# Performance work log

Hardware: AMD Instinct MI355X
Metric: run time of the kernel (lower is better)

## Reference

```python
import jax, jax.numpy as jnp
import numpy as np

# Dimensions (babyGPT-50m: GPT-2-small-ish)
B, T, V, C, H, L = 2, 1024, 50257, 768, 12, 6
D = C // H
STD = 0.02
EPS = 1e-5


def _normal(k, shape):
    return (jax.random.normal(k, shape, dtype=jnp.float32) * STD)


def setup_inputs() -> dict:
    key = jax.random.key(0)
    ks = jax.random.split(key, 12)
    inp = {
        "idx": jax.random.randint(ks[0], (B, T), 0, V, dtype=jnp.int64 if jax.config.jax_enable_x64 else jnp.int32),
        "tok_emb": _normal(ks[1], (V, C)),
        "pos_emb": _normal(ks[2], (1, T, C)),
        # per-layer params stacked along leading L axis
        "ln1_g": jnp.ones((L, C), jnp.float32),
        "ln1_b": jnp.zeros((L, C), jnp.float32),
        "Wq": _normal(ks[3], (L, C, C)), "bq": jnp.zeros((L, C), jnp.float32),
        "Wk": _normal(ks[4], (L, C, C)), "bk": jnp.zeros((L, C), jnp.float32),
        "Wv": _normal(ks[5], (L, C, C)), "bv": jnp.zeros((L, C), jnp.float32),
        "Wp": _normal(ks[6], (L, C, C)), "bp": jnp.zeros((L, C), jnp.float32),
        "ln2_g": jnp.ones((L, C), jnp.float32),
        "ln2_b": jnp.zeros((L, C), jnp.float32),
        "Wf1": _normal(ks[7], (L, C, 4 * C)), "bf1": jnp.zeros((L, 4 * C), jnp.float32),
        "Wf2": _normal(ks[8], (L, 4 * C, C)), "bf2": jnp.zeros((L, C), jnp.float32),
        "lnf_g": jnp.ones((C,), jnp.float32),
        "lnf_b": jnp.zeros((C,), jnp.float32),
        "head_W": _normal(ks[9], (C, V)),  # head has bias=False
    }
    return inp


def _ln(x, g, b):
    m = jnp.mean(x, axis=-1, keepdims=True)
    v = jnp.var(x, axis=-1, keepdims=True)
    return (x - m) * jax.lax.rsqrt(v + EPS) * g + b


def _gpt_forward(idx, tok_emb, pos_emb, ln1_g, ln1_b, Wq, bq, Wk, bk, Wv, bv,
                 Wp, bp, ln2_g, ln2_b, Wf1, bf1, Wf2, bf2, lnf_g, lnf_b, head_W):
    x = tok_emb[idx] + pos_emb[:, :T]          # [B,T,C]; dropout is identity (eval)
    causal = jnp.tril(jnp.ones((T, T), bool))  # same tril mask as the buffer
    scale = 1.0 / np.sqrt(D).astype(np.float32)

    def block(x, p):
        g1, b1, wq, bq_, wk, bk_, wv, bv_, wp, bp_, g2, b2, w1, b1f, w2, b2f = p
        h = _ln(x, g1, b1)
        q = (h @ wq + bq_).reshape(B, T, H, D)
        k = (h @ wk + bk_).reshape(B, T, H, D)
        v = (h @ wv + bv_).reshape(B, T, H, D)
        att = jnp.einsum('bthd,bshd->bhts', q, k) * scale   # [B,H,T,T]
        att = jnp.where(causal, att, jnp.float32(-10000.0))  # masked_fill value
        att = jax.nn.softmax(att, axis=-1)
        y = jnp.einsum('bhts,bshd->bthd', att, v).reshape(B, T, C)
        x = x + y @ wp + bp_
        h2 = _ln(x, g2, b2)
        ff = jax.nn.gelu(h2 @ w1 + b1f, approximate=False) @ w2 + b2f  # exact GELU, dropout=eval
        return x + ff, None

    layer_params = (ln1_g, ln1_b, Wq, bq, Wk, bk, Wv, bv, Wp, bp,
                    ln2_g, ln2_b, Wf1, bf1, Wf2, bf2)
    x, _ = jax.lax.scan(block, x, layer_params)
    x = _ln(x, lnf_g, lnf_b)
    return x @ head_W  # logits [B,T,V]


def reference(idx, tok_emb, pos_emb, ln1_g, ln1_b, Wq, bq, Wk, bk, Wv, bv,
              Wp, bp, ln2_g, ln2_b, Wf1, bf1, Wf2, bf2, lnf_g, lnf_b, head_W):
    return _gpt_forward(idx, tok_emb, pos_emb, ln1_g, ln1_b, Wq, bq, Wk, bk, Wv, bv,
                        Wp, bp, ln2_g, ln2_b, Wf1, bf1, Wf2, bf2, lnf_g, lnf_b, head_W)
```

## Files before the change

kernel.cpp:

```cpp
#include <hip/hip_runtime.h>
#include <hip/hip_bf16.h>
#include <math.h>

#define Bsz 2
#define Tt 1024
#define Vv 50257
#define Cc 768
#define Hh 12
#define Ll 6
#define NTOK (Bsz*Tt)
#define VPAD 50304

typedef __attribute__((ext_vector_type(8))) short bf16x8;
typedef __attribute__((ext_vector_type(8))) unsigned short u16x8;
typedef __attribute__((ext_vector_type(4))) unsigned short u16x4;
typedef __attribute__((ext_vector_type(4))) float f32x4;
typedef unsigned short u16;

static __device__ __forceinline__ u16 f2bf(float f){
  unsigned u = __float_as_uint(f);
  u += 0x7FFF + ((u >> 16) & 1);
  return (u16)(u >> 16);
}
static __device__ __forceinline__ float bf2f(u16 h){
  return __uint_as_float(((unsigned)h) << 16);
}

#define GL16(g,l) __builtin_amdgcn_global_load_lds( \
    (const __attribute__((address_space(1))) void*)(g), \
    (__attribute__((address_space(3))) void*)(l), 16, 0, 0)
#define WAITVM(n) asm volatile("s_waitcnt vmcnt(%0)" :: "n"(n) : "memory")

__global__ void embed_kernel(const int* __restrict__ idx, const float* __restrict__ tok,
                             const float* __restrict__ pos, float* __restrict__ x){
  const int C4 = Cc/4;
  int i = blockIdx.x * 256 + threadIdx.x;
  if (i >= NTOK*C4) return;
  int tk = i / C4, c4 = i % C4;
  int row = idx[tk];
  int t = tk % Tt;
  float4 a = ((const float4*)tok)[(size_t)row*C4 + c4];
  float4 p = ((const float4*)pos)[(size_t)t*C4 + c4];
  float4 r; r.x=a.x+p.x; r.y=a.y+p.y; r.z=a.z+p.z; r.w=a.w+p.w;
  ((float4*)x)[i] = r;
}

__global__ void ln_kernel(const float* __restrict__ in, const float* __restrict__ g,
                          const float* __restrict__ bt, u16* __restrict__ out){
  int row = blockIdx.x, tid = threadIdx.x;
  const float* r = in + (size_t)row*Cc;
  float v0=r[tid], v1=r[tid+256], v2=r[tid+512];
  float s  = v0+v1+v2;
  float s2 = v0*v0+v1*v1+v2*v2;
  #pragma unroll
  for (int off=32; off; off>>=1){ s += __shfl_xor(s,off); s2 += __shfl_xor(s2,off); }
  __shared__ float red[8];
  int wid = tid >> 6;
  if ((tid & 63) == 0){ red[wid]=s; red[4+wid]=s2; }
  __syncthreads();
  float S  = red[0]+red[1]+red[2]+red[3];
  float S2 = red[4]+red[5]+red[6]+red[7];
  float mean = S * (1.0f/Cc);
  float var  = S2 * (1.0f/Cc) - mean*mean;
  float rstd = rsqrtf(var + 1e-5f);
  u16* o = out + (size_t)row*Cc;
  o[tid]     = f2bf((v0-mean)*rstd*g[tid]     + bt[tid]);
  o[tid+256] = f2bf((v1-mean)*rstd*g[tid+256] + bt[tid+256]);
  o[tid+512] = f2bf((v2-mean)*rstd*g[tid+512] + bt[tid+512]);
}

__global__ void wtrans_kernel(const float* __restrict__ in, u16* __restrict__ out,
                              int K, int N, int Npad, size_t lsi, size_t lso){
  __shared__ u16 t[64][68];
  const float* inp = in + (size_t)blockIdx.z*lsi;
  u16* op = out + (size_t)blockIdx.z*lso;
  int n0 = blockIdx.x*64, k0 = blockIdx.y*64;
  int tid = threadIdx.x;
  #pragma unroll
  for (int i=0;i<4;i++){
    int e = tid + 256*i;
    int k = e >> 4, n4 = (e & 15) * 4;
    int n = n0 + n4;
    const float* rowp = inp + (size_t)(k0+k)*N;
    float4 v;
    if (n + 3 < N) v = *(const float4*)&rowp[n];
    else {
      v.x = (n   < N) ? rowp[n  ] : 0.f;
      v.y = (n+1 < N) ? rowp[n+1] : 0.f;
      v.z = (n+2 < N) ? rowp[n+2] : 0.f;
      v.w = (n+3 < N) ? rowp[n+3] : 0.f;
    }
    u16x4 pk; pk[0]=f2bf(v.x); pk[1]=f2bf(v.y); pk[2]=f2bf(v.z); pk[3]=f2bf(v.w);
    *(u16x4*)&t[k][n4] = pk;
  }
  __syncthreads();
  #pragma unroll
  for (int i=0;i<2;i++){
    int e = tid + 256*i;
    int n = e >> 3, k8 = (e & 7) * 8;
    u16x8 pk;
    #pragma unroll
    for (int q=0;q<8;q++) pk[q] = t[k8+q][n];
    if (n0 + n < Npad)
      *(u16x8*)&op[(size_t)(n0+n)*K + k0 + k8] = pk;
  }
}

__global__ void vtrans_kernel(const u16* __restrict__ qkv, u16* __restrict__ vT){
  __shared__ u16 s[32][33];
  int bh = blockIdx.z; int b = bh/Hh, h = bh - b*Hh;
  int t0 = blockIdx.x*32, d0 = blockIdx.y*32;
  int tx=threadIdx.x, ty=threadIdx.y;
  #pragma unroll
  for (int i=0;i<4;i++)
    s[ty+i*8][tx] = qkv[(size_t)(b*Tt + t0+ty+i*8)*2304 + 1536 + h*64 + d0 + tx];
  __syncthreads();
  #pragma unroll
  for (int i=0;i<4;i++)
    vT[((size_t)bh*64 + d0+ty+i*8)*Tt + t0 + tx] = s[tx][ty+i*8];
}

__global__ void bconcat_kernel(const float* __restrict__ bq, const float* __restrict__ bk,
                               const float* __restrict__ bv, float* __restrict__ o){
  int i = blockIdx.x*256 + threadIdx.x;
  if (i >= Ll*2304) return;
  int l = i/2304, j = i - l*2304;
  o[i] = (j < 768) ? bq[l*768+j] : (j < 1536) ? bk[l*768+j-768] : bv[l*768+j-1536];
}

__global__ __launch_bounds__(256) void flash_kernel(
    const u16* __restrict__ qkv, const u16* __restrict__ vT, u16* __restrict__ y){
  __shared__ u16 Ks[2][64*64];
  __shared__ u16 Vs[2][64*64];
  __shared__ u16 Ps[4][16*64];
  int bx = blockIdx.x;
  int bh = blockIdx.y; int b = bh/Hh, h = bh - b*Hh;
  int q0 = bx*64;
  int tid = threadIdx.x, lane = tid&63, wid = tid>>6;
  const size_t tokbase = (size_t)b*Tt;
  int arow = lane&15, akof = (lane>>4)*8;
  bf16x8 qa[2];
  #pragma unroll
  for (int ks=0;ks<2;ks++)
    qa[ks] = *(const bf16x8*)&qkv[(tokbase + q0 + wid*16 + arow)*2304
                                  + h*64 + ks*32 + akof];
  int srow = lane>>3;
  int sbyte = ((lane&7)*16) ^ (srow<<4);
  const u16* kbase = qkv + tokbase*2304 + 768 + h*64;
  const u16* vbase = vT + (size_t)bh*64*Tt;
  auto STAGEKV = [&](int t, int bb){
    int j0 = t*64;
    #pragma unroll
    for (int c=0;c<2;c++){
      int r = wid*16 + c*8 + srow;
      GL16(kbase + (size_t)(j0 + r)*2304 + (sbyte>>1), &Ks[bb][(wid*16 + c*8)*64]);
      GL16(vbase + (size_t)r*Tt + j0 + (sbyte>>1),     &Vs[bb][(wid*16 + c*8)*64]);
    }
  };
  float m_r[4], l_r[4];
  f32x4 o_acc[4] = {};
  #pragma unroll
  for (int jj=0;jj<4;jj++){ m_r[jj] = -1e30f; l_r[jj] = 0.f; }

  int njt = bx + 1;
  STAGEKV(0, 0);
  asm volatile("s_waitcnt vmcnt(0)" ::: "memory");
  __builtin_amdgcn_s_barrier();
  for (int t=0; t<njt; t++){
    int cur = t&1;
    if (t+1 < njt) STAGEKV(t+1, cur^1);
    int j0 = t*64;
    f32x4 sacc[4] = {};
    #pragma unroll
    for (int ks=0;ks<2;ks++){
      bf16x8 kf[4];
      #pragma unroll
      for (int ni=0;ni<4;ni++){
        int s16 = ni*16 + (lane&15);
        int kb = (ks*64 + (lane>>4)*16) ^ ((s16&7)<<4);
        kf[ni] = *(const bf16x8*)((const char*)&Ks[cur][0] + s16*128 + kb);
      }
      #pragma unroll
      for (int ni=0;ni<4;ni++)
        sacc[ni] = __builtin_amdgcn_mfma_f32_16x16x32_bf16(qa[ks], kf[ni], sacc[ni], 0,0,0);
    }
    float tmax[4];
    #pragma unroll
    for (int jj=0;jj<4;jj++) tmax[jj] = -1e30f;
    #pragma unroll
    for (int ni=0;ni<4;ni++)
      #pragma unroll
      for (int jj=0;jj<4;jj++){
        float v = sacc[ni][jj]*0.125f;
        int sg = j0 + ni*16 + (lane&15);
        int tg = q0 + wid*16 + (lane>>4)*4 + jj;
        v = (sg <= tg) ? v : -1e30f;
        sacc[ni][jj] = v;
        tmax[jj] = fmaxf(tmax[jj], v);
      }
    #pragma unroll
    for (int jj=0;jj<4;jj++){
      float tm = tmax[jj];
      tm = fmaxf(tm, __shfl_xor(tm,1)); tm = fmaxf(tm, __shfl_xor(tm,2));
      tm = fmaxf(tm, __shfl_xor(tm,4)); tm = fmaxf(tm, __shfl_xor(tm,8));
      float mn = fmaxf(m_r[jj], tm);
      float al = __expf(m_r[jj] - mn);
      m_r[jj] = mn;
      l_r[jj] *= al;
      tmax[jj] = al;
    }
    float tsum[4] = {};
    #pragma unroll
    for (int ni=0;ni<4;ni++)
      #pragma unroll
      for (int jj=0;jj<4;jj++){
        float p = __expf(sacc[ni][jj] - m_r[jj]);
        tsum[jj] += p;
        int pr = (lane>>4)*4 + jj;
        int pcb = (2*(ni*16 + (lane&15))) ^ ((pr&7)<<4);
        *(u16*)((char*)&Ps[wid][0] + pr*128 + pcb) = f2bf(p);
      }
    #pragma unroll
    for (int jj=0;jj<4;jj++){
      float ts = tsum[jj];
      ts += __shfl_xor(ts,1); ts += __shfl_xor(ts,2);
      ts += __shfl_xor(ts,4); ts += __shfl_xor(ts,8);
      l_r[jj] += ts;
      float al = tmax[jj];
      #pragma unroll
      for (int ni2=0;ni2<4;ni2++) o_acc[ni2][jj] *= al;
    }
    #pragma unroll
    for (int ks2=0;ks2<2;ks2++){
      bf16x8 pa, vf[4];
      int prr = lane&15;
      int pb = (ks2*64 + (lane>>4)*16) ^ ((prr&7)<<4);
      pa = *(const bf16x8*)((const char*)&Ps[wid][0] + prr*128 + pb);
      #pragma unroll
      for (int ni2=0;ni2<4;ni2++){
        int d16 = ni2*16 + (lane&15);
        int sb = (ks2*64 + (lane>>4)*16) ^ ((d16&7)<<4);
        vf[ni2] = *(const bf16x8*)((const char*)&Vs[cur][0] + d16*128 + sb);
      }
      #pragma unroll
      for (int ni2=0;ni2<4;ni2++)
        o_acc[ni2] = __builtin_amdgcn_mfma_f32_16x16x32_bf16(pa, vf[ni2], o_acc[ni2], 0,0,0);
    }
    asm volatile("s_waitcnt vmcnt(0) lgkmcnt(0)" ::: "memory");
    __builtin_amdgcn_s_barrier();
  }
  #pragma unroll
  for (int jj=0;jj<4;jj++){
    float inv = 1.0f / l_r[jj];
    int tok2 = q0 + wid*16 + (lane>>4)*4 + jj;
    size_t rb = (tokbase + tok2)*Cc + h*64;
    #pragma unroll
    for (int ni2=0;ni2<4;ni2++)
      y[rb + ni2*16 + (lane&15)] = f2bf(o_acc[ni2][jj] * inv);
  }
}

template<int NBUF, int NTHR, int WN, int BM, int BN, int BK,
         bool BIAS, bool RESID, bool GELU, bool OUTBF, bool ROWSCAN>
__global__ __launch_bounds__(NTHR) void mm_kernel(
    const u16* __restrict__ A, const u16* __restrict__ Bm,
    const float* __restrict__ bias, const float* __restrict__ resid,
    void* __restrict__ out, int N, int K, int lda, int ldb, int ldc)
{
  constexpr int WAVES = NTHR/64;
  constexpr int WM    = WAVES/WN;
  constexpr int FM    = BM/(WM*16);
  constexpr int FN    = BN/(WN*16);
  constexpr int KSTEPS = BK/32;
  constexpr int CPW   = FN*16;
  constexpr int ESTR  = CPW + 4;
  constexpr int ABUF  = BM*BK;
  constexpr int BBUF  = BN*BK;
  constexpr int ARPW  = BM/WAVES;
  constexpr int BRPW  = BN/WAVES;
  constexpr int RPC   = (BK==64) ? 8 : 16;
  constexpr int ACALLS = ARPW/RPC;
  constexpr int BCALLS = BRPW/RPC;
  constexpr int LOADS = ACALLS + BCALLS;
  constexpr int SMEM_STAGE = NBUF*(ABUF+BBUF)*2;
  constexpr int SMEM_EPI   = WAVES*16*ESTR*4;
  constexpr int SMEMB = SMEM_STAGE > SMEM_EPI ? SMEM_STAGE : SMEM_EPI;
  __shared__ __align__(16) char smem[SMEMB];
  u16* As = (u16*)smem;
  u16* Bs = As + NBUF*ABUF;

  int bx = blockIdx.x, by = blockIdx.y;
  {
    int gx = gridDim.x;
    int nwg = gx * gridDim.y;
    int flat = by*gx + bx;
    int qq = nwg >> 3, rr = nwg & 7;
    int xcd = flat & 7, lid = flat >> 3;
    int swz = (xcd < rr) ? xcd*(qq+1) + lid : rr*(qq+1) + (xcd-rr)*qq + lid;
    bx = swz % gx; by = swz / gx;
  }
  int m0 = bx*BM, n0 = by*BN;
  int tid = threadIdx.x, lane = tid & 63, wid = tid >> 6;
  int r0 = (wid/WN)*(BM/WM), c0 = (wid%WN)*(BN/WN);
  int lrow = lane & 15;
  int rl, sswz;
  if constexpr (BK==64){ rl = lane>>3; sswz = ((lane&7) ^ (lane>>3)) * 8; }
  else                 { rl = lane>>2; sswz = ((lane&3) ^ ((lane>>3)&3)) * 8; }
  const u16* Ap = A + (size_t)(m0 + wid*ARPW + rl)*lda + sswz;
  const u16* Bp = Bm + (size_t)(n0 + wid*BRPW + rl)*ldb + sswz;
  int nt = K/BK;
  auto STAGE = [&](int t, int bb){
    int kk = t*BK;
    u16* Al = As + bb*ABUF + (wid*ARPW)*BK;
    #pragma unroll
    for (int c=0;c<ACALLS;c++)
      GL16(Ap + kk + (size_t)(c*RPC)*lda, Al + c*512);
    u16* Bl = Bs + bb*BBUF + (wid*BRPW)*BK;
    #pragma unroll
    for (int c=0;c<BCALLS;c++)
      GL16(Bp + kk + (size_t)(c*RPC)*ldb, Bl + c*512);
  };
  f32x4 acc[FM][FN] = {};
  if constexpr (NBUF==2){
    STAGE(0, 0);
    WAITVM(0);
    __builtin_amdgcn_s_barrier();
  } else {
    STAGE(0, 0);
    if (nt > 1) STAGE(1, 1);
    WAITVM(LOADS);
    __builtin_amdgcn_s_barrier();
  }
  for (int t = 0; t < nt; t++){
    int bb = (NBUF==2) ? (t & 1) : (t % 3);
    if constexpr (NBUF==2){
      if (t+1 < nt) STAGE(t+1, (t+1)&1);
    } else {
      if (t+2 < nt) STAGE(t+2, (t+2)%3);
    }
    const char* Ab2 = (const char*)(As + bb*ABUF);
    const char* Bb2 = (const char*)(Bs + bb*BBUF);
    #pragma unroll
    for (int ks=0;ks<KSTEPS;ks++){
      int cof;
      if constexpr (BK==64) cof = ((ks*4 + (lane>>4)) ^ (lane&7)) << 4;
      else                  cof = ((lane>>4) ^ (((lane&15)>>1)&3)) << 4;
      bf16x8 af[FM], bfr[FN];
      #pragma unroll
      for (int m=0;m<FM;m++) af[m] = *(const bf16x8*)(Ab2 + (r0 + m*16 + lrow)*(BK*2) + cof);
      #pragma unroll
      for (int n=0;n<FN;n++) bfr[n] = *(const bf16x8*)(Bb2 + (c0 + n*16 + lrow)*(BK*2) + cof);
      #pragma unroll
      for (int m=0;m<FM;m++)
        #pragma unroll
        for (int n=0;n<FN;n++)
          acc[m][n] = __builtin_amdgcn_mfma_f32_16x16x32_bf16(af[m], bfr[n], acc[m][n], 0,0,0);
    }
    if constexpr (NBUF==2){
      asm volatile("s_waitcnt vmcnt(0) lgkmcnt(0)" ::: "memory");
    } else {
      if (t+2 < nt) WAITVM(LOADS); else WAITVM(0);
    }
    __builtin_amdgcn_s_barrier();
  }

  float* ebuf = (float*)smem + wid*16*ESTR;
  int er = lane >> 2;
  int ec = (lane & 3) * (CPW/4);
  #pragma unroll
  for (int m=0;m<FM;m++){
    #pragma unroll
    for (int n=0;n<FN;n++)
      #pragma unroll
      for (int j=0;j<4;j++)
        ebuf[((lane>>4)*4+j)*ESTR + n*16 + (lane&15)] = acc[m][n][j];
    __builtin_amdgcn_s_waitcnt(0);
    if constexpr (ROWSCAN){
      #pragma unroll
      for (int rr2=0; rr2<16; rr2++){
        int gr2 = m0 + r0 + m*16 + rr2;
        int gc2 = n0 + c0 + lane;
        float v = ebuf[rr2*ESTR + lane];
        if (gc2 < N)
          __builtin_nontemporal_store(v, &((float*)out)[(size_t)gr2*ldc + gc2]);
      }
    } else {
      int grow = m0 + r0 + m*16 + er;
      int gcol = n0 + c0 + ec;
      size_t rbase = (size_t)grow*ldc;
      if constexpr (OUTBF){
        u16 tmp[CPW/4];
        #pragma unroll
        for (int q=0;q<FN;q++){
          float4 v = *(const float4*)&ebuf[er*ESTR + ec + q*4];
          float f0=v.x, f1=v.y, f2=v.z, f3=v.w;
          if (BIAS){
            float4 b4 = *(const float4*)&bias[gcol + q*4];
            f0+=b4.x; f1+=b4.y; f2+=b4.z; f3+=b4.w;
          }
          if (GELU){
            f0 = 0.5f*f0*(1.f+erff(f0*0.70710678118654752f));
            f1 = 0.5f*f1*(1.f+erff(f1*0.70710678118654752f));
            f2 = 0.5f*f2*(1.f+erff(f2*0.70710678118654752f));
            f3 = 0.5f*f3*(1.f+erff(f3*0.70710678118654752f));
          }
          tmp[q*4+0]=f2bf(f0); tmp[q*4+1]=f2bf(f1);
          tmp[q*4+2]=f2bf(f2); tmp[q*4+3]=f2bf(f3);
        }
        #pragma unroll
        for (int s2=0; s2<CPW/32; s2++)
          *(u16x8*)&((u16*)out)[rbase + gcol + s2*8] = *(const u16x8*)&tmp[s2*8];
      } else {
        #pragma unroll
        for (int q=0;q<FN;q++){
          float4 v = *(const float4*)&ebuf[er*ESTR + ec + q*4];
          float f0=v.x, f1=v.y, f2=v.z, f3=v.w;
          if (BIAS){
            float4 b4 = *(const float4*)&bias[gcol + q*4];
            f0+=b4.x; f1+=b4.y; f2+=b4.z; f3+=b4.w;
          }
          if (GELU){
            f0 = 0.5f*f0*(1.f+erff(f0*0.70710678118654752f));
            f1 = 0.5f*f1*(1.f+erff(f1*0.70710678118654752f));
            f2 = 0.5f*f2*(1.f+erff(f2*0.70710678118654752f));
            f3 = 0.5f*f3*(1.f+erff(f3*0.70710678118654752f));
          }
          if (RESID){
            float4 r4 = *(const float4*)&resid[rbase + gcol + q*4];
            f0+=r4.x; f1+=r4.y; f2+=r4.z; f3+=r4.w;
          }
          float4 o4; o4.x=f0; o4.y=f1; o4.z=f2; o4.w=f3;
          *(float4*)&((float*)out)[rbase + gcol + q*4] = o4;
        }
      }
    }
  }
}

extern "C" void kernel_launch(void* const* d_in, const int* in_sizes, int n_in,
                              void* d_out, int out_size, void* d_ws, size_t ws_size,
                              hipStream_t stream){
  const int*   idx  = (const int*)d_in[0];
  const float* tok  = (const float*)d_in[1];
  const float* pos  = (const float*)d_in[2];
  const float* ln1g = (const float*)d_in[3];
  const float* ln1b = (const float*)d_in[4];
  const float* Wq   = (const float*)d_in[5];
  const float* bq   = (const float*)d_in[6];
  const float* Wk   = (const float*)d_in[7];
  const float* bk   = (const float*)d_in[8];
  const float* Wv   = (const float*)d_in[9];
  const float* bv   = (const float*)d_in[10];
  const float* Wp   = (const float*)d_in[11];
  const float* bp   = (const float*)d_in[12];
  const float* ln2g = (const float*)d_in[13];
  const float* ln2b = (const float*)d_in[14];
  const float* Wf1  = (const float*)d_in[15];
  const float* bf1  = (const float*)d_in[16];
  const float* Wf2  = (const float*)d_in[17];
  const float* bf2  = (const float*)d_in[18];
  const float* lnfg = (const float*)d_in[19];
  const float* lnfb = (const float*)d_in[20];
  const float* headW= (const float*)d_in[21];
  float* outp = (float*)d_out;

  char* w = (char*)d_ws;
  u16* wqkvT = (u16*)w;  w += (size_t)Ll*2304*768*2;
  u16* wpT   = (u16*)w;  w += (size_t)Ll*768*768*2;
  u16* wf1T  = (u16*)w;  w += (size_t)Ll*3072*768*2;
  u16* wf2T  = (u16*)w;  w += (size_t)Ll*768*3072*2;
  u16* headT = (u16*)w;  w += (size_t)VPAD*768*2;
  float* bqkv= (float*)w;w += (size_t)Ll*2304*4;
  float* x   = (float*)w;w += (size_t)NTOK*Cc*4;
  u16* h     = (u16*)w;  w += (size_t)NTOK*Cc*2;
  u16* qkv   = (u16*)w;  w += (size_t)NTOK*2304*2;
  u16* vT    = (u16*)w;  w += (size_t)Bsz*Hh*64*Tt*2;
  u16* y     = (u16*)w;  w += (size_t)NTOK*Cc*2;
  u16* ff    = (u16*)w;  w += (size_t)NTOK*4*Cc*2;

  dim3 tb(32,8);
  wtrans_kernel<<<dim3(12,12,Ll), 256, 0, stream>>>(Wq, wqkvT,          768, 768, 768, (size_t)Cc*Cc, (size_t)2304*768);
  wtrans_kernel<<<dim3(12,12,Ll), 256, 0, stream>>>(Wk, wqkvT+768*768,  768, 768, 768, (size_t)Cc*Cc, (size_t)2304*768);
  wtrans_kernel<<<dim3(12,12,Ll), 256, 0, stream>>>(Wv, wqkvT+1536*768, 768, 768, 768, (size_t)Cc*Cc, (size_t)2304*768);
  wtrans_kernel<<<dim3(12,12,Ll), 256, 0, stream>>>(Wp, wpT,            768, 768, 768, (size_t)Cc*Cc, (size_t)768*768);
  wtrans_kernel<<<dim3(48,12,Ll), 256, 0, stream>>>(Wf1, wf1T,          768, 3072, 3072, (size_t)Cc*4*Cc, (size_t)3072*768);
  wtrans_kernel<<<dim3(12,48,Ll), 256, 0, stream>>>(Wf2, wf2T,          3072, 768, 768, (size_t)4*Cc*Cc, (size_t)768*3072);
  wtrans_kernel<<<dim3(VPAD/64,12,1), 256, 0, stream>>>(headW, headT, 768, Vv, VPAD, 0, 0);
  bconcat_kernel<<<(Ll*2304+255)/256, 256, 0, stream>>>(bq, bk, bv, bqkv);

  embed_kernel<<<NTOK*(Cc/4)/256, 256, 0, stream>>>(idx, tok, pos, x);

  for (int l=0;l<Ll;l++){
    ln_kernel<<<NTOK, 256, 0, stream>>>(x, ln1g+l*Cc, ln1b+l*Cc, h);
    mm_kernel<2,256,2,64,128,64,true,false,false,true,false><<<dim3(32,18,1), 256, 0, stream>>>(
        h, wqkvT+(size_t)l*2304*768, bqkv+l*2304, nullptr, qkv, 2304, 768, 768, 768, 2304);
    vtrans_kernel<<<dim3(32,2,Bsz*Hh), tb, 0, stream>>>(qkv, vT);
    flash_kernel<<<dim3(Tt/64, Bsz*Hh), 256, 0, stream>>>(qkv, vT, y);
    mm_kernel<3,256,2,64,64,64,true,true,false,false,false><<<dim3(32,12,1), 256, 0, stream>>>(
        y, wpT+(size_t)l*768*768, bp+l*Cc, x, x, 768, 768, 768, 768, 768);
    ln_kernel<<<NTOK, 256, 0, stream>>>(x, ln2g+l*Cc, ln2b+l*Cc, h);
    mm_kernel<2,256,2,64,128,64,true,false,true,true,false><<<dim3(32,24,1), 256, 0, stream>>>(
        h, wf1T+(size_t)l*3072*768, bf1+(size_t)l*4*Cc, nullptr, ff, 3072, 768, 768, 768, 3072);
    mm_kernel<3,256,2,64,64,64,true,true,false,false,false><<<dim3(32,12,1), 256, 0, stream>>>(
        ff, wf2T+(size_t)l*768*3072, bf2+l*Cc, x, x, 768, 3072, 3072, 3072, 768);
  }
  ln_kernel<<<NTOK, 256, 0, stream>>>(x, lnfg, lnfb, h);
  mm_kernel<2,256,2,128,128,32,false,false,false,false,true><<<dim3(16,VPAD/128,1), 256, 0, stream>>>(
      h, headT, nullptr, nullptr, outp, Vv, 768, 768, 768, Vv);
}
```

Before: 1.097 ms.

## Add dedicated LM-head GEMM kernel with 256x128 tiles and interleaved MFMA/load schedule

Replaces the generic mm_kernel for the vocabulary projection with a specialized 512-thread kernel using 256x128 tiles, triple-buffered LDS, XOR-swizzled shared-memory layout and an XCD-aware workgroup remapping. Each K-step is split into four phases that interleave LDS fragment reads, global prefetch chunks and MFMA bursts with setprio to overlap memory and math. The head GEMM is the largest single matmul, so this targets its throughput, at the cost of many barriers per iteration and higher register and LDS use. The ROWSCAN template path is removed from mm_kernel since only the head used it.

```diff
diff --git a/kernel.cpp b/kernel.cpp
--- a/kernel.cpp
+++ b/kernel.cpp
@@ -260,8 +260,160 @@
   }
 }
 
+__global__ __launch_bounds__(512) void mmhead_kernel(
+    const u16* __restrict__ A, const u16* __restrict__ Bm,
+    float* __restrict__ out, int N, int K, int lda, int ldb, int ldc)
+{
+  __shared__ __align__(16) u16 smem[3*16384 + 3*8192];
+  u16* As = smem;
+  u16* Bs = smem + 3*16384;
+  int bx = blockIdx.x, by = blockIdx.y;
+  {
+    int gx = gridDim.x;
+    int nwg = gx * gridDim.y;
+    int flat = by*gx + bx;
+    int qq = nwg >> 3, rr = nwg & 7;
+    int xcd = flat & 7, lid = flat >> 3;
+    int swz = (xcd < rr) ? xcd*(qq+1) + lid : rr*(qq+1) + (xcd-rr)*qq + lid;
+    bx = swz % gx; by = swz / gx;
+  }
+  int m0 = bx*256, n0 = by*128;
+  int tid = threadIdx.x, lane = tid & 63, wid = tid >> 6;
+  int wr = wid >> 1, wc = wid & 1;
+  int r0 = wr*64, c0 = wc*64;
+  int lrow = lane & 15;
+  int sswz = ((lane & 7) ^ (lane >> 3)) * 8;
+  const u16* Ap = A + (size_t)(m0 + wid*32 + (lane>>3))*lda + sswz;
+  const u16* Bp = Bm + (size_t)(n0 + wid*16 + (lane>>3))*ldb + sswz;
+  int cof0 = (((lane>>4)    ) ^ (lane&7)) << 4;
+  int cof1 = (((lane>>4) + 4) ^ (lane&7)) << 4;
+  const int nt = K/64;
+  f32x4 acc[4][4] = {};
+
+  #pragma unroll
+  for (int c=0;c<4;c++) GL16(Ap + (size_t)(c*8)*lda,      As + (wid*32 + c*8)*64);
+  #pragma unroll
+  for (int c=0;c<2;c++) GL16(Bp + (size_t)(c*8)*ldb,      Bs + (wid*16 + c*8)*64);
+  #pragma unroll
+  for (int c=0;c<4;c++) GL16(Ap + 64 + (size_t)(c*8)*lda, As + 16384 + (wid*32 + c*8)*64);
+  #pragma unroll
+  for (int c=0;c<2;c++) GL16(Bp + 64 + (size_t)(c*8)*ldb, Bs + 8192  + (wid*16 + c*8)*64);
+  WAITVM(6);
+  __builtin_amdgcn_s_barrier();
+
+  for (int t = 0; t < nt; t++){
+    int s = t % 3;
+    const char* Ab = (const char*)(As + s*16384);
+    const char* Bb = (const char*)(Bs + s*8192);
+    bool st = (t+2 < nt);
+    int s2 = (t+2) % 3;
+    const u16* Ap2 = Ap + (t+2)*64;
+    const u16* Bp2 = Bp + (t+2)*64;
+    u16* Al2 = As + s2*16384 + (wid*32)*64;
+    u16* Bl2 = Bs + s2*8192  + (wid*16)*64;
+    bf16x8 afA[2][2], afB[2][2], bfr[4][2];
+
+    #pragma unroll
+    for (int m=0;m<2;m++){
+      afA[m][0] = *(const bf16x8*)(Ab + (r0 + m*16 + lrow)*128 + cof0);
+      afA[m][1] = *(const bf16x8*)(Ab + (r0 + m*16 + lrow)*128 + cof1);
+    }
+    #pragma unroll
+    for (int n=0;n<2;n++){
+      bfr[n][0] = *(const bf16x8*)(Bb + (c0 + n*16 + lrow)*128 + cof0);
+      bfr[n][1] = *(const bf16x8*)(Bb + (c0 + n*16 + lrow)*128 + cof1);
+    }
+    if (st){ GL16(Ap2, Al2); GL16(Ap2 + (size_t)8*lda, Al2 + 512); }
+    __builtin_amdgcn_s_barrier();
+    asm volatile("s_waitcnt lgkmcnt(0)" ::: "memory");
+    __builtin_amdgcn_sched_barrier(0);
+    __builtin_amdgcn_s_setprio(1);
+    #pragma unroll
+    for (int m=0;m<2;m++)
+      #pragma unroll
+      for (int n=0;n<2;n++){
+        acc[m][n] = __builtin_amdgcn_mfma_f32_16x16x32_bf16(afA[m][0], bfr[n][0], acc[m][n], 0,0,0);
+        acc[m][n] = __builtin_amdgcn_mfma_f32_16x16x32_bf16(afA[m][1], bfr[n][1], acc[m][n], 0,0,0);
+      }
+    __builtin_amdgcn_s_setprio(0);
+    __builtin_amdgcn_s_barrier();
+
+    #pragma unroll
+    for (int n=2;n<4;n++){
+      bfr[n][0] = *(const bf16x8*)(Bb + (c0 + n*16 + lrow)*128 + cof0);
+      bfr[n][1] = *(const bf16x8*)(Bb + (c0 + n*16 + lrow)*128 + cof1);
+    }
+    if (st){ GL16(Ap2 + (size_t)16*lda, Al2 + 1024); GL16(Ap2 + (size_t)24*lda, Al2 + 1536); }
+    __builtin_amdgcn_s_barrier();
+    asm volatile("s_waitcnt lgkmcnt(0)" ::: "memory");
+    __builtin_amdgcn_sched_barrier(0);
+    __builtin_amdgcn_s_setprio(1);
+    #pragma unroll
+    for (int m=0;m<2;m++)
+      #pragma unroll
+      for (int n=2;n<4;n++){
+        acc[m][n] = __builtin_amdgcn_mfma_f32_16x16x32_bf16(afA[m][0], bfr[n][0], acc[m][n], 0,0,0);
+        acc[m][n] = __builtin_amdgcn_mfma_f32_16x16x32_bf16(afA[m][1], bfr[n][1], acc[m][n], 0,0,0);
+      }
+    __builtin_amdgcn_s_setprio(0);
+    __builtin_amdgcn_s_barrier();
+
+    #pragma unroll
+    for (int m=0;m<2;m++){
+      afB[m][0] = *(const bf16x8*)(Ab + (r0 + 32 + m*16 + lrow)*128 + cof0);
+      afB[m][1] = *(const bf16x8*)(Ab + (r0 + 32 + m*16 + lrow)*128 + cof1);
+    }
+    if (st){ GL16(Bp2, Bl2); GL16(Bp2 + (size_t)8*ldb, Bl2 + 512); }
+    __builtin_amdgcn_s_barrier();
+    asm volatile("s_waitcnt lgkmcnt(0)" ::: "memory");
+    __builtin_amdgcn_sched_barrier(0);
+    __builtin_amdgcn_s_setprio(1);
+    #pragma unroll
+    for (int m=0;m<2;m++)
+      #pragma unroll
+      for (int n=0;n<2;n++){
+        acc[2+m][n] = __builtin_amdgcn_mfma_f32_16x16x32_bf16(afB[m][0], bfr[n][0], acc[2+m][n], 0,0,0);
+        acc[2+m][n] = __builtin_amdgcn_mfma_f32_16x16x32_bf16(afB[m][1], bfr[n][1], acc[2+m][n], 0,0,0);
+      }
+    __builtin_amdgcn_s_setprio(0);
+    __builtin_amdgcn_s_barrier();
+
+    __builtin_amdgcn_s_setprio(1);
+    #pragma unroll
+    for (int m=0;m<2;m++)
+      #pragma unroll
+      for (int n=2;n<4;n++){
+        acc[2+m][n] = __builtin_amdgcn_mfma_f32_16x16x32_bf16(afB[m][0], bfr[n][0], acc[2+m][n], 0,0,0);
+        acc[2+m][n] = __builtin_amdgcn_mfma_f32_16x16x32_bf16(afB[m][1], bfr[n][1], acc[2+m][n], 0,0,0);
+      }
+    __builtin_amdgcn_s_setprio(0);
+    if (st) { WAITVM(6); } else { WAITVM(0); }
+    __builtin_amdgcn_s_barrier();
+  }
+
+  constexpr int ESTR = 68;
+  float* ebuf = (float*)smem + wid*16*ESTR;
+  #pragma unroll
+  for (int m=0;m<4;m++){
+    #pragma unroll
+    for (int n=0;n<4;n++)
+      #pragma unroll
+      for (int j=0;j<4;j++)
+        ebuf[((lane>>4)*4+j)*ESTR + n*16 + (lane&15)] = acc[m][n][j];
+    __builtin_amdgcn_s_waitcnt(0);
+    #pragma unroll
+    for (int rr2=0; rr2<16; rr2++){
+      int gr2 = m0 + r0 + m*16 + rr2;
+      int gc2 = n0 + c0 + lane;
+      float v = ebuf[rr2*ESTR + lane];
+      if (gc2 < N)
+        __builtin_nontemporal_store(v, &out[(size_t)gr2*ldc + gc2]);
+    }
+  }
+}
+
 template<int NBUF, int NTHR, int WN, int BM, int BN, int BK,
-         bool BIAS, bool RESID, bool GELU, bool OUTBF, bool ROWSCAN>
+         bool BIAS, bool RESID, bool GELU, bool OUTBF>
 __global__ __launch_bounds__(NTHR) void mm_kernel(
     const u16* __restrict__ A, const u16* __restrict__ Bm,
     const float* __restrict__ bias, const float* __restrict__ resid,
@@ -375,63 +527,52 @@
       for (int j=0;j<4;j++)
         ebuf[((lane>>4)*4+j)*ESTR + n*16 + (lane&15)] = acc[m][n][j];
     __builtin_amdgcn_s_waitcnt(0);
-    if constexpr (ROWSCAN){
-      #pragma unroll
-      for (int rr2=0; rr2<16; rr2++){
-        int gr2 = m0 + r0 + m*16 + rr2;
-        int gc2 = n0 + c0 + lane;
-        float v = ebuf[rr2*ESTR + lane];
-        if (gc2 < N)
-          __builtin_nontemporal_store(v, &((float*)out)[(size_t)gr2*ldc + gc2]);
-      }
+    int grow = m0 + r0 + m*16 + er;
+    int gcol = n0 + c0 + ec;
+    size_t rbase = (size_t)grow*ldc;
+    if constexpr (OUTBF){
+      u16 tmp[CPW/4];
+      #pragma unroll
+      for (int q=0;q<FN;q++){
+        float4 v = *(const float4*)&ebuf[er*ESTR + ec + q*4];
+        float f0=v.x, f1=v.y, f2=v.z, f3=v.w;
+        if (BIAS){
+          float4 b4 = *(const float4*)&bias[gcol + q*4];
+          f0+=b4.x; f1+=b4.y; f2+=b4.z; f3+=b4.w;
+        }
+        if (GELU){
+          f0 = 0.5f*f0*(1.f+erff(f0*0.70710678118654752f));
+          f1 = 0.5f*f1*(1.f+erff(f1*0.70710678118654752f));
+          f2 = 0.5f*f2*(1.f+erff(f2*0.70710678118654752f));
+          f3 = 0.5f*f3*(1.f+erff(f3*0.70710678118654752f));
+        }
+        tmp[q*4+0]=f2bf(f0); tmp[q*4+1]=f2bf(f1);
+        tmp[q*4+2]=f2bf(f2); tmp[q*4+3]=f2bf(f3);
+      }
+      #pragma unroll
+      for (int s2=0; s2<CPW/32; s2++)
+        *(u16x8*)&((u16*)out)[rbase + gcol + s2*8] = *(const u16x8*)&tmp[s2*8];
     } else {
-      int grow = m0 + r0 + m*16 + er;
-      int gcol = n0 + c0 + ec;
-      size_t rbase = (size_t)grow*ldc;
-      if constexpr (OUTBF){
-        u16 tmp[CPW/4];
-        #pragma unroll
-        for (int q=0;q<FN;q++){
-          float4 v = *(const float4*)&ebuf[er*ESTR + ec + q*4];
-          float f0=v.x, f1=v.y, f2=v.z, f3=v.w;
-          if (BIAS){
-            float4 b4 = *(const float4*)&bias[gcol + q*4];
-            f0+=b4.x; f1+=b4.y; f2+=b4.z; f3+=b4.w;
-          }
-          if (GELU){
-            f0 = 0.5f*f0*(1.f+erff(f0*0.70710678118654752f));
-            f1 = 0.5f*f1*(1.f+erff(f1*0.70710678118654752f));
-            f2 = 0.5f*f2*(1.f+erff(f2*0.70710678118654752f));
-            f3 = 0.5f*f3*(1.f+erff(f3*0.70710678118654752f));
-          }
-          tmp[q*4+0]=f2bf(f0); tmp[q*4+1]=f2bf(f1);
-          tmp[q*4+2]=f2bf(f2); tmp[q*4+3]=f2bf(f3);
+      #pragma unroll
+      for (int q=0;q<FN;q++){
+        float4 v = *(const float4*)&ebuf[er*ESTR + ec + q*4];
+        float f0=v.x, f1=v.y, f2=v.z, f3=v.w;
+        if (BIAS){
+          float4 b4 = *(const float4*)&bias[gcol + q*4];
+          f0+=b4.x; f1+=b4.y; f2+=b4.z; f3+=b4.w;
         }
-        #pragma unroll
-        for (int s2=0; s2<CPW/32; s2++)
-          *(u16x8*)&((u16*)out)[rbase + gcol + s2*8] = *(const u16x8*)&tmp[s2*8];
-      } else {
-        #pragma unroll
-        for (int q=0;q<FN;q++){
-          float4 v = *(const float4*)&ebuf[er*ESTR + ec + q*4];
-          float f0=v.x, f1=v.y, f2=v.z, f3=v.w;
-          if (BIAS){
-            float4 b4 = *(const float4*)&bias[gcol + q*4];
-            f0+=b4.x; f1+=b4.y; f2+=b4.z; f3+=b4.w;
-          }
-          if (GELU){
-            f0 = 0.5f*f0*(1.f+erff(f0*0.70710678118654752f));
-            f1 = 0.5f*f1*(1.f+erff(f1*0.70710678118654752f));
-            f2 = 0.5f*f2*(1.f+erff(f2*0.70710678118654752f));
-            f3 = 0.5f*f3*(1.f+erff(f3*0.70710678118654752f));
-          }
-          if (RESID){
-            float4 r4 = *(const float4*)&resid[rbase + gcol + q*4];
-            f0+=r4.x; f1+=r4.y; f2+=r4.z; f3+=r4.w;
-          }
-          float4 o4; o4.x=f0; o4.y=f1; o4.z=f2; o4.w=f3;
-          *(float4*)&((float*)out)[rbase + gcol + q*4] = o4;
+        if (GELU){
+          f0 = 0.5f*f0*(1.f+erff(f0*0.70710678118654752f));
+          f1 = 0.5f*f1*(1.f+erff(f1*0.70710678118654752f));
+          f2 = 0.5f*f2*(1.f+erff(f2*0.70710678118654752f));
+          f3 = 0.5f*f3*(1.f+erff(f3*0.70710678118654752f));
         }
+        if (RESID){
+          float4 r4 = *(const float4*)&resid[rbase + gcol + q*4];
+          f0+=r4.x; f1+=r4.y; f2+=r4.z; f3+=r4.w;
+        }
+        float4 o4; o4.x=f0; o4.y=f1; o4.z=f2; o4.w=f3;
+        *(float4*)&((float*)out)[rbase + gcol + q*4] = o4;
       }
     }
   }
@@ -492,19 +633,19 @@
 
   for (int l=0;l<Ll;l++){
     ln_kernel<<<NTOK, 256, 0, stream>>>(x, ln1g+l*Cc, ln1b+l*Cc, h);
-    mm_kernel<2,256,2,64,128,64,true,false,false,true,false><<<dim3(32,18,1), 256, 0, stream>>>(
+    mm_kernel<2,256,2,64,128,64,true,false,false,true><<<dim3(32,18,1), 256, 0, stream>>>(
         h, wqkvT+(size_t)l*2304*768, bqkv+l*2304, nullptr, qkv, 2304, 768, 768, 768, 2304);
     vtrans_kernel<<<dim3(32,2,Bsz*Hh), tb, 0, stream>>>(qkv, vT);
     flash_kernel<<<dim3(Tt/64, Bsz*Hh), 256, 0, stream>>>(qkv, vT, y);
-    mm_kernel<3,256,2,64,64,64,true,true,false,false,false><<<dim3(32,12,1), 256, 0, stream>>>(
+    mm_kernel<3,256,2,64,64,64,true,true,false,false><<<dim3(32,12,1), 256, 0, stream>>>(
         y, wpT+(size_t)l*768*768, bp+l*Cc, x, x, 768, 768, 768, 768, 768);
     ln_kernel<<<NTOK, 256, 0, stream>>>(x, ln2g+l*Cc, ln2b+l*Cc, h);
-    mm_kernel<2,256,2,64,128,64,true,false,true,true,false><<<dim3(32,24,1), 256, 0, stream>>>(
+    mm_kernel<2,256,2,64,128,64,true,false,true,true><<<dim3(32,24,1), 256, 0, stream>>>(
         h, wf1T+(size_t)l*3072*768, bf1+(size_t)l*4*Cc, nullptr, ff, 3072, 768, 768, 768, 3072);
-    mm_kernel<3,256,2,64,64,64,true,true,false,false,false><<<dim3(32,12,1), 256, 0, stream>>>(
+    mm_kernel<3,256,2,64,64,64,true,true,false,false><<<dim3(32,12,1), 256, 0, stream>>>(
         ff, wf2T+(size_t)l*768*3072, bf2+l*Cc, x, x, 768, 3072, 3072, 3072, 768);
   }
   ln_kernel<<<NTOK, 256, 0, stream>>>(x, lnfg, lnfb, h);
-  mm_kernel<2,256,2,128,128,32,false,false,false,false,true><<<dim3(16,VPAD/128,1), 256, 0, stream>>>(
-      h, headT, nullptr, nullptr, outp, Vv, 768, 768, 768, Vv);
-}
+  mmhead_kernel<<<dim3(NTOK/256, VPAD/128, 1), 512, 0, stream>>>(
+      h, headT, outp, Vv, 768, 768, 768, Vv);
+}
```

Measured after the change: 1.148 ms. 1.05x slower.
